# Kernel tuning notes

Hardware: AMD Instinct MI355X
Metric: run time of the kernel (lower is better)

## Reference

```python
import jax, jax.numpy as jnp
import numpy as np

V, D, H, L, T_MAX = 50257, 1024, 16, 12, 256
HS = D // H
B, T = 8, 256


def setup_inputs() -> dict:
    key = jax.random.key(0)
    ks = jax.random.split(key, 24)
    s = 0.02
    inp = {
        'idx': jax.random.randint(ks[0], (B, T), 0, V),
        'targets': jax.random.randint(ks[1], (B, T), 0, V),
        'tok_emb': jax.random.normal(ks[2], (V, D), jnp.float32) * s,
        'pos_emb': jax.random.normal(ks[3], (T_MAX, D), jnp.float32) * s,
        'Wq': jax.random.normal(ks[4], (L, H, D, HS), jnp.float32) / np.sqrt(D),
        'Wk': jax.random.normal(ks[5], (L, H, D, HS), jnp.float32) / np.sqrt(D),
        'Wv': jax.random.normal(ks[6], (L, H, D, HS), jnp.float32) / np.sqrt(D),
        'ln1_g': jnp.ones((L, D), jnp.float32),
        'ln1_b': jnp.zeros((L, D), jnp.float32),
        'ln2_g': jnp.ones((L, D), jnp.float32),
        'ln2_b': jnp.zeros((L, D), jnp.float32),
        'fc1_w': jax.random.normal(ks[7], (L, D, 4 * D), jnp.float32) / np.sqrt(D),
        'fc1_b': jnp.zeros((L, 4 * D), jnp.float32),
        'fc2_w': jax.random.normal(ks[8], (L, 4 * D, D), jnp.float32) / np.sqrt(4 * D),
        'fc2_b': jnp.zeros((L, D), jnp.float32),
        'lnf_g': jnp.ones((D,), jnp.float32),
        'lnf_b': jnp.zeros((D,), jnp.float32),
        'lm_w': jax.random.normal(ks[9], (D, V), jnp.float32) / np.sqrt(D),
        'lm_b': jnp.zeros((V,), jnp.float32),
    }
    return inp


def _layernorm(x, g, b, eps=1e-5):
    mu = jnp.mean(x, axis=-1, keepdims=True)
    var = jnp.var(x, axis=-1, keepdims=True)
    return (x - mu) * jax.lax.rsqrt(var + eps) * g + b


def reference(idx, targets, tok_emb, pos_emb, Wq, Wk, Wv, ln1_g, ln1_b, ln2_g, ln2_b,
              fc1_w, fc1_b, fc2_w, fc2_b, lnf_g, lnf_b, lm_w, lm_b):
    Bc, Tc = idx.shape
    x = tok_emb[idx] + pos_emb[:Tc]  # [B,T,D]
    causal = jnp.tril(jnp.ones((Tc, Tc), bool))
    scale = 1.0 / np.sqrt(HS)
    for l in range(L):
        h = _layernorm(x, ln1_g[l], ln1_b[l])
        q = jnp.einsum('btd,hds->bhts', h, Wq[l])
        k = jnp.einsum('btd,hds->bhts', h, Wk[l])
        v = jnp.einsum('btd,hds->bhts', h, Wv[l])
        scores = jnp.einsum('bhts,bhus->bhtu', q, k) * scale
        scores = jnp.where(causal, scores, -jnp.inf)
        attn = jax.nn.softmax(scores, axis=-1)
        o = jnp.einsum('bhtu,bhus->bhts', attn, v)  # [B,H,T,hs]
        o = o.transpose(0, 2, 1, 3).reshape(Bc, Tc, D)  # concat heads
        x = x + o  # no output projection in original
        h = _layernorm(x, ln2_g[l], ln2_b[l])
        ff = jax.nn.relu(h @ fc1_w[l] + fc1_b[l]) @ fc2_w[l] + fc2_b[l]
        x = x + ff
    x = _layernorm(x, lnf_g, lnf_b)
    logits = x @ lm_w + lm_b  # [B,T,V]
    logp = jax.nn.log_softmax(logits, axis=-1)
    nll = -jnp.take_along_axis(logp, targets[..., None], axis=-1)[..., 0]
    loss = jnp.mean(nll)
    return logits, loss
```

## Files before the change

### kernel.cpp

```cpp
#include <hip/hip_runtime.h>

#define T_SEQ 256
#define DMODEL 1024
#define NHEAD 16
#define HSZ 64
#define NLAYER 12
#define VOCAB 50257
#define NPAD 50304
#define FF 4096
#define MROWS 2048

using short8 = __attribute__((ext_vector_type(8))) short;
using f32x4  = __attribute__((ext_vector_type(4))) float;

__device__ __forceinline__ float bf2f(unsigned short u) {
    unsigned int x = ((unsigned int)u) << 16;
    return __builtin_bit_cast(float, x);
}
__device__ __forceinline__ unsigned short f2bf(float f) {
    unsigned int u = __builtin_bit_cast(unsigned int, f);
    unsigned int r = (u + 0x7fffu + ((u >> 16) & 1u)) >> 16;
    return (unsigned short)r;
}
__device__ __forceinline__ void async_copy16(const void* g, void* l) {
    __builtin_amdgcn_global_load_lds(
        (const __attribute__((address_space(1))) unsigned int*)g,
        (__attribute__((address_space(3))) unsigned int*)l, 16, 0, 0);
}

__device__ __forceinline__ void ln_tail(
    float4 v, const float* __restrict__ g, const float* __restrict__ b,
    int row, int tid, unsigned short* __restrict__ out)
{
    float s  = v.x + v.y + v.z + v.w;
    float ss = v.x * v.x + v.y * v.y + v.z * v.z + v.w * v.w;
    for (int o = 32; o > 0; o >>= 1) {
        s  += __shfl_down(s, o);
        ss += __shfl_down(ss, o);
    }
    __shared__ float ps[4], pss[4];
    int wave = tid >> 6, lane = tid & 63;
    if (lane == 0) { ps[wave] = s; pss[wave] = ss; }
    __syncthreads();
    float st  = ps[0] + ps[1] + ps[2] + ps[3];
    float sst = pss[0] + pss[1] + pss[2] + pss[3];
    float mu  = st * (1.0f / DMODEL);
    float var = sst * (1.0f / DMODEL) - mu * mu;
    float rstd = rsqrtf(var + 1e-5f);
    float4 gv = ((const float4*)g)[tid];
    float4 bv = ((const float4*)b)[tid];
    ushort4 o4;
    o4.x = f2bf((v.x - mu) * rstd * gv.x + bv.x);
    o4.y = f2bf((v.y - mu) * rstd * gv.y + bv.y);
    o4.z = f2bf((v.z - mu) * rstd * gv.z + bv.z);
    o4.w = f2bf((v.w - mu) * rstd * gv.w + bv.w);
    ((ushort4*)out)[(size_t)row * (DMODEL / 4) + tid] = o4;
}

__global__ __launch_bounds__(256) void embed_ln_kernel(
    const int* __restrict__ idx, const float* __restrict__ tok,
    const float* __restrict__ pos, const float* __restrict__ g,
    const float* __restrict__ b, float* __restrict__ x,
    unsigned short* __restrict__ h)
{
    int row = blockIdx.x, tid = threadIdx.x;
    int t = row & (T_SEQ - 1);
    int token = idx[row];
    float4 a = ((const float4*)(tok + (size_t)token * DMODEL))[tid];
    float4 p = ((const float4*)(pos + (size_t)t * DMODEL))[tid];
    float4 v;
    v.x = a.x + p.x; v.y = a.y + p.y; v.z = a.z + p.z; v.w = a.w + p.w;
    ((float4*)(x + (size_t)row * DMODEL))[tid] = v;
    ln_tail(v, g, b, row, tid, h);
}

__global__ __launch_bounds__(256) void ln_kernel(
    const float* __restrict__ x, const float* __restrict__ g,
    const float* __restrict__ b, unsigned short* __restrict__ out)
{
    int row = blockIdx.x, tid = threadIdx.x;
    float4 v = ((const float4*)(x + (size_t)row * DMODEL))[tid];
    ln_tail(v, g, b, row, tid, out);
}

__global__ __launch_bounds__(256) void fc2_merge_ln_kernel(
    const float* __restrict__ part, const float* __restrict__ bias,
    const float* __restrict__ g, const float* __restrict__ b,
    float* __restrict__ x, unsigned short* __restrict__ h)
{
    int row = blockIdx.x, tid = threadIdx.x;
    size_t o = (size_t)row * (DMODEL / 4) + tid;
    float4 p0 = ((const float4*)part)[o];
    float4 p1 = ((const float4*)part)[o + MROWS * (DMODEL / 4)];
    float4 bv = ((const float4*)bias)[tid];
    float4 v = ((float4*)x)[o];
    v.x += p0.x + p1.x + bv.x;
    v.y += p0.y + p1.y + bv.y;
    v.z += p0.z + p1.z + bv.z;
    v.w += p0.w + p1.w + bv.w;
    ((float4*)x)[o] = v;
    ln_tail(v, g, b, row, tid, h);
}

__global__ __launch_bounds__(256) void wtranspose_kernel(
    const float* __restrict__ in, unsigned short* __restrict__ out,
    int R, int C, int Cout, long in_l, long out_l)
{
    int lyr = blockIdx.z;
    in  += (size_t)lyr * in_l;
    out += (size_t)lyr * out_l;
    __shared__ float tile[32][33];
    int tx = threadIdx.x & 31, ty = threadIdx.x >> 5;
    int c0 = blockIdx.x * 32, r0 = blockIdx.y * 32;
    #pragma unroll
    for (int i = 0; i < 4; i++) {
        int r = r0 + ty + i * 8, c = c0 + tx;
        tile[ty + i * 8][tx] = (c < C) ? in[(size_t)r * C + c] : 0.f;
    }
    __syncthreads();
    #pragma unroll
    for (int i = 0; i < 4; i++) {
        int c = c0 + ty + i * 8, r = r0 + tx;
        if (c < Cout) out[(size_t)c * R + r] = f2bf(tile[tx][ty + i * 8]);
    }
}

__global__ __launch_bounds__(256) void qkvpack_kernel(
    const float* __restrict__ Wq, const float* __restrict__ Wk,
    const float* __restrict__ Wv, unsigned short* __restrict__ out,
    long w_l, long out_l)
{
    int z = blockIdx.z;
    int lyr = z / 48, r48 = z % 48;
    int seg = r48 >> 4, hh = r48 & 15;
    const float* W = (seg == 0 ? Wq : seg == 1 ? Wk : Wv)
                     + (size_t)lyr * w_l + (size_t)hh * DMODEL * HSZ;
    unsigned short* o = out + (size_t)lyr * out_l
                      + (size_t)(seg * 1024 + hh * 64) * DMODEL;
    __shared__ float tile[32][33];
    int tx = threadIdx.x & 31, ty = threadIdx.x >> 5;
    int d0 = blockIdx.x * 32, s0 = blockIdx.y * 32;
    #pragma unroll
    for (int i = 0; i < 4; i++)
        tile[ty + i * 8][tx] = W[(size_t)(d0 + ty + i * 8) * HSZ + s0 + tx];
    __syncthreads();
    #pragma unroll
    for (int i = 0; i < 4; i++)
        o[(size_t)(s0 + ty + i * 8) * DMODEL + d0 + tx] = f2bf(tile[tx][ty + i * 8]);
}

template<int MF, int WAVES, bool QKV, bool RELU, bool RES, bool CBF16>
__device__ __forceinline__ void gemm_core(
    const unsigned short* __restrict__ A, int lda,
    const unsigned short* __restrict__ Bt, int ldb,
    const float* __restrict__ bias,
    void* __restrict__ Cv, int ldc,
    const float* __restrict__ res, int ldr,
    int N, int K,
    unsigned short* __restrict__ vtout)
{
    constexpr int BM = (WAVES / 2) * MF * 16;
    constexpr int BJ = 16 / WAVES;
    __shared__ __align__(16) char As[BM * 128];
    __shared__ __align__(16) char Bs[128 * 128];
    int tid = threadIdx.x;
    int wave = tid >> 6, lane = tid & 63;
    int wr = wave >> 1, wc = wave & 1;
    int m0 = blockIdx.x * BM, n0 = blockIdx.y * 128;

    f32x4 acc[MF][4];
    #pragma unroll
    for (int m = 0; m < MF; m++)
        #pragma unroll
        for (int n = 0; n < 4; n++)
            acc[m][n] = (f32x4){0.f, 0.f, 0.f, 0.f};

    int ksw = (((lane & 7) ^ (lane >> 3)) << 4);
    int KT = K >> 6;
    for (int kt = 0; kt < KT; kt++) {
        int k0 = kt << 6;
        __syncthreads();
        #pragma unroll
        for (int j = 0; j < MF; j++) {
            int row = (wave * MF + j) * 8 + (lane >> 3);
            const char* src = (const char*)A + ((size_t)(m0 + row) * lda + k0) * 2 + ksw;
            async_copy16(src, As + (wave * MF + j) * 1024);
        }
        #pragma unroll
        for (int j = 0; j < BJ; j++) {
            int nrow = (wave * BJ + j) * 8 + (lane >> 3);
            const char* src = (const char*)Bt + ((size_t)(n0 + nrow) * ldb + k0) * 2 + ksw;
            async_copy16(src, Bs + (wave * BJ + j) * 1024);
        }
        __syncthreads();
        #pragma unroll
        for (int ks = 0; ks < 2; ks++) {
            int kb = ks * 64 + ((lane >> 4) << 4);
            short8 a[MF], b[4];
            #pragma unroll
            for (int m = 0; m < MF; m++) {
                int r = wr * (MF * 16) + m * 16 + (lane & 15);
                a[m] = *(const short8*)(const void*)(As + r * 128 + (kb ^ ((r & 7) << 4)));
            }
            #pragma unroll
            for (int n = 0; n < 4; n++) {
                int c = wc * 64 + n * 16 + (lane & 15);
                b[n] = *(const short8*)(const void*)(Bs + c * 128 + (kb ^ ((c & 7) << 4)));
            }
            #pragma unroll
            for (int m = 0; m < MF; m++)
                #pragma unroll
                for (int n = 0; n < 4; n++)
                    acc[m][n] = __builtin_amdgcn_mfma_f32_16x16x32_bf16(a[m], b[n], acc[m][n], 0, 0, 0);
        }
    }
    #pragma unroll
    for (int m = 0; m < MF; m++) {
        int rowb = m0 + wr * (MF * 16) + m * 16 + ((lane >> 4) << 2);
        #pragma unroll
        for (int n = 0; n < 4; n++) {
            int col = n0 + wc * 64 + n * 16 + (lane & 15);
            if (col < N) {
                float bi = bias ? bias[col] : 0.f;
                #pragma unroll
                for (int r2 = 0; r2 < 4; r2++) {
                    float v = acc[m][n][r2] + bi;
                    if (RELU) v = fmaxf(v, 0.f);
                    int row = rowb + r2;
                    if (RES) v += res[(size_t)row * ldr + col];
                    if (QKV && col >= 2048) {
                        int hh = (col - 2048) >> 6, sdim = (col - 2048) & 63;
                        int bb = row >> 8, tt = row & 255;
                        vtout[((((size_t)bb * NHEAD + hh) * HSZ + sdim) * T_SEQ) + tt] = f2bf(v);
                    } else if (CBF16) {
                        ((unsigned short*)Cv)[(size_t)row * ldc + col] = f2bf(v);
                    } else {
                        ((float*)Cv)[(size_t)row * ldc + col] = v;
                    }
                }
            }
        }
    }
}

__global__ __launch_bounds__(256) void gemm_qkv(
    const unsigned short* __restrict__ A, const unsigned short* __restrict__ Bt,
    unsigned short* __restrict__ C, unsigned short* __restrict__ vtout)
{
    gemm_core<4, 4, true, false, false, true>(
        A, DMODEL, Bt, DMODEL, nullptr, C, 3072, nullptr, 0, 3072, DMODEL, vtout);
}

__global__ __launch_bounds__(256) void gemm_fc1(
    const unsigned short* __restrict__ A, const unsigned short* __restrict__ Bt,
    const float* __restrict__ bias, unsigned short* __restrict__ C)
{
    gemm_core<4, 4, false, true, false, true>(
        A, DMODEL, Bt, DMODEL, bias, C, FF, nullptr, 0, FF, DMODEL, nullptr);
}

__global__ __launch_bounds__(256) void gemm_fc2(
    const unsigned short* __restrict__ A, const unsigned short* __restrict__ Bt,
    float* __restrict__ part)
{
    int z = blockIdx.z;
    gemm_core<2, 4, false, false, false, false>(
        A + z * 2048, FF, Bt + z * 2048, FF, nullptr,
        part + (size_t)z * MROWS * DMODEL, DMODEL, nullptr, 0,
        DMODEL, 2048, nullptr);
}

__global__ __launch_bounds__(512) void gemm_lm(
    const unsigned short* __restrict__ A, const unsigned short* __restrict__ Bt,
    const float* __restrict__ bias, float* __restrict__ C)
{
    gemm_core<4, 8, false, false, false, false>(
        A, DMODEL, Bt, DMODEL, bias, C, VOCAB, nullptr, 0, VOCAB, DMODEL, nullptr);
}

__global__ __launch_bounds__(256) void attn_fused_kernel(
    const unsigned short* __restrict__ qkv, const unsigned short* __restrict__ vt,
    float* __restrict__ x)
{
    int qt = blockIdx.x, hh = blockIdx.y, b = blockIdx.z;
    int tid = threadIdx.x;
    int wave = tid >> 6, lane = tid & 63;
    int g = lane >> 4, q = lane & 15;

    __shared__ __align__(16) char Kb[2][8192];
    __shared__ __align__(16) char Vb[2][8192];
    __shared__ __align__(16) char Plds[4][2048];

    int qrow = b * T_SEQ + qt * 64 + wave * 16 + q;
    const char* qp = (const char*)qkv + ((size_t)qrow * 3072 + hh * HSZ) * 2;
    short8 qreg[2];
    qreg[0] = *(const short8*)(const void*)(qp + (g << 4));
    qreg[1] = *(const short8*)(const void*)(qp + 64 + (g << 4));

    char* Pw = Plds[wave];

    f32x4 oacc[4];
    #pragma unroll
    for (int f = 0; f < 4; f++) oacc[f] = (f32x4){0.f, 0.f, 0.f, 0.f};
    float m_run = -1e30f, l_run = 0.f;

    int srow = wave * 8 + (lane >> 3);
    int sbyte = ((lane & 7) << 4) ^ ((srow & 7) << 4);

    auto stage = [&](int kt, int bi) {
        #pragma unroll
        for (int c = 0; c < 2; c++) {
            int row = c * 32 + srow;
            const char* src = (const char*)qkv +
                ((size_t)(b * T_SEQ + kt * 64 + row) * 3072 + 1024 + hh * HSZ) * 2 + sbyte;
            async_copy16(src, Kb[bi] + c * 4096 + wave * 1024);
        }
        #pragma unroll
        for (int c = 0; c < 2; c++) {
            int row = c * 32 + srow;
            const char* src = (const char*)vt +
                (((size_t)(b * NHEAD + hh) * HSZ + row) * T_SEQ + kt * 64) * 2 + sbyte;
            async_copy16(src, Vb[bi] + c * 4096 + wave * 1024);
        }
    };

    stage(0, 0);
    for (int kt = 0; kt <= qt; kt++) {
        int bi = kt & 1;
        __syncthreads();
        if (kt < qt) stage(kt + 1, bi ^ 1);

        f32x4 sacc[4];
        #pragma unroll
        for (int f = 0; f < 4; f++) sacc[f] = (f32x4){0.f, 0.f, 0.f, 0.f};
        #pragma unroll
        for (int ks = 0; ks < 2; ks++) {
            int kb = ks * 64 + (g << 4);
            #pragma unroll
            for (int f = 0; f < 4; f++) {
                int u = f * 16 + q;
                short8 kf = *(const short8*)(const void*)(Kb[bi] + u * 128 + (kb ^ ((u & 7) << 4)));
                sacc[f] = __builtin_amdgcn_mfma_f32_16x16x32_bf16(kf, qreg[ks], sacc[f], 0, 0, 0);
            }
        }
        float sv[4][4];
        #pragma unroll
        for (int f = 0; f < 4; f++)
            #pragma unroll
            for (int r = 0; r < 4; r++) {
                float v = sacc[f][r] * 0.125f;
                if (kt == qt) {
                    int u_loc = f * 16 + g * 4 + r;
                    if (u_loc > wave * 16 + q) v = -1e30f;
                }
                sv[f][r] = v;
            }
        float pm = -1e30f;
        #pragma unroll
        for (int f = 0; f < 4; f++)
            #pragma unroll
            for (int r = 0; r < 4; r++) pm = fmaxf(pm, sv[f][r]);
        pm = fmaxf(pm, __shfl_xor(pm, 16));
        pm = fmaxf(pm, __shfl_xor(pm, 32));
        float mnew = fmaxf(m_run, pm);
        float corr = __expf(m_run - mnew);
        float p[4][4];
        float ls = 0.f;
        #pragma unroll
        for (int f = 0; f < 4; f++)
            #pragma unroll
            for (int r = 0; r < 4; r++) {
                p[f][r] = __expf(sv[f][r] - mnew);
                ls += p[f][r];
            }
        ls += __shfl_xor(ls, 16);
        ls += __shfl_xor(ls, 32);
        l_run = l_run * corr + ls;
        m_run = mnew;
        #pragma unroll
        for (int r = 0; r < 4; r++) {
            float cr = __shfl(corr, (lane & 48) | (g * 4 + r));
            #pragma unroll
            for (int f = 0; f < 4; f++) oacc[f][r] *= cr;
        }
        #pragma unroll
        for (int f = 0; f < 4; f++)
            #pragma unroll
            for (int rp = 0; rp < 2; rp++) {
                int ue = f * 16 + g * 4 + rp * 2;
                unsigned int pk = (unsigned int)f2bf(p[f][rp * 2])
                                | ((unsigned int)f2bf(p[f][rp * 2 + 1]) << 16);
                *(unsigned int*)(void*)(Pw + q * 128 + ((ue * 2) ^ ((q & 7) << 4))) = pk;
            }
        #pragma unroll
        for (int ks = 0; ks < 2; ks++) {
            int kb = ks * 64 + (g << 4);
            short8 pa = *(const short8*)(const void*)(Pw + q * 128 + (kb ^ ((q & 7) << 4)));
            #pragma unroll
            for (int f = 0; f < 4; f++) {
                int s = f * 16 + q;
                short8 vf = *(const short8*)(const void*)(Vb[bi] + s * 128 + (kb ^ ((s & 7) << 4)));
                oacc[f] = __builtin_amdgcn_mfma_f32_16x16x32_bf16(pa, vf, oacc[f], 0, 0, 0);
            }
        }
    }
    float inv = 1.0f / l_run;
    #pragma unroll
    for (int r = 0; r < 4; r++) {
        float ir = __shfl(inv, (lane & 48) | (g * 4 + r));
        int row_g = b * T_SEQ + qt * 64 + wave * 16 + g * 4 + r;
        #pragma unroll
        for (int f = 0; f < 4; f++) {
            size_t xi = (size_t)row_g * DMODEL + hh * HSZ + f * 16 + q;
            x[xi] += oacc[f][r] * ir;
        }
    }
}

__global__ __launch_bounds__(256) void loss1_kernel(
    const float* __restrict__ logits, const int* __restrict__ targets,
    float* __restrict__ nll)
{
    int r = blockIdx.x, tid = threadIdx.x;
    const float* row = logits + (size_t)r * VOCAB;
    const float4* row4 = (const float4*)row;
    float m = -3.4e38f, s = 0.f;
    for (int v = tid; v < VOCAB / 4; v += 256) {
        float4 x4 = row4[v];
        float lm = fmaxf(fmaxf(x4.x, x4.y), fmaxf(x4.z, x4.w));
        float nm = fmaxf(m, lm);
        s = s * __expf(m - nm) + __expf(x4.x - nm) + __expf(x4.y - nm)
          + __expf(x4.z - nm) + __expf(x4.w - nm);
        m = nm;
    }
    if (tid == 0) {
        float xv = row[VOCAB - 1];
        float nm = fmaxf(m, xv);
        s = s * __expf(m - nm) + __expf(xv - nm);
        m = nm;
    }
    __shared__ float ms[256], ssh[256];
    ms[tid] = m; ssh[tid] = s;
    __syncthreads();
    for (int o = 128; o > 0; o >>= 1) {
        if (tid < o) {
            float m1 = ms[tid], s1 = ssh[tid];
            float m2 = ms[tid + o], s2 = ssh[tid + o];
            float nm = fmaxf(m1, m2);
            ssh[tid] = s1 * __expf(m1 - nm) + s2 * __expf(m2 - nm);
            ms[tid] = nm;
        }
        __syncthreads();
    }
    if (tid == 0) nll[r] = logf(ssh[0]) + ms[0] - row[targets[r]];
}

__global__ __launch_bounds__(256) void loss2_kernel(
    const float* __restrict__ nll, float* __restrict__ out)
{
    int tid = threadIdx.x;
    float s = 0.f;
    for (int i = tid; i < MROWS; i += 256) s += nll[i];
    __shared__ float red[256];
    red[tid] = s;
    __syncthreads();
    for (int o = 128; o > 0; o >>= 1) {
        if (tid < o) red[tid] += red[tid + o];
        __syncthreads();
    }
    if (tid == 0) out[0] = red[0] * (1.0f / MROWS);
}

extern "C" void kernel_launch(void* const* d_in, const int* in_sizes, int n_in,
                              void* d_out, int out_size, void* d_ws, size_t ws_size,
                              hipStream_t stream)
{
    const int*   idx  = (const int*)d_in[0];
    const int*   tgt  = (const int*)d_in[1];
    const float* tok  = (const float*)d_in[2];
    const float* pos  = (const float*)d_in[3];
    const float* Wq   = (const float*)d_in[4];
    const float* Wk   = (const float*)d_in[5];
    const float* Wv   = (const float*)d_in[6];
    const float* ln1g = (const float*)d_in[7];
    const float* ln1b = (const float*)d_in[8];
    const float* ln2g = (const float*)d_in[9];
    const float* ln2b = (const float*)d_in[10];
    const float* fc1w = (const float*)d_in[11];
    const float* fc1b = (const float*)d_in[12];
    const float* fc2w = (const float*)d_in[13];
    const float* fc2b = (const float*)d_in[14];
    const float* lnfg = (const float*)d_in[15];
    const float* lnfb = (const float*)d_in[16];
    const float* lmw  = (const float*)d_in[17];
    const float* lmb  = (const float*)d_in[18];

    char* ws = (char*)d_ws;
    float*          x    = (float*)(ws + 0);
    unsigned short* h    = (unsigned short*)(ws + 8388608);
    unsigned short* qkv  = (unsigned short*)(ws + 12582912);
    unsigned short* vt   = (unsigned short*)(ws + 25165824);
    unsigned short* mid  = (unsigned short*)(ws + 29360128);
    float*          nll  = (float*)(ws + 46137344);
    float*          fc2p = (float*)(ws + 46145536);
    unsigned short* lmwt = (unsigned short*)(ws + 62922752);
    const size_t UP_NEED = 442769408ull;
    bool upfront = (ws_size >= UP_NEED);
    unsigned short* qkvt = (unsigned short*)(ws + 165945344);
    unsigned short* fc1t, * fc2t;
    long qkvt_l, fc1t_l, fc2t_l;
    if (upfront) {
        fc1t = (unsigned short*)(ws + 241442816);
        fc2t = (unsigned short*)(ws + 342106112);
        qkvt_l = 3072 * 1024; fc1t_l = (long)FF * 1024; fc2t_l = (long)1024 * FF;
    } else {
        fc1t = (unsigned short*)(ws + 172236800);
        fc2t = (unsigned short*)(ws + 180625408);
        qkvt_l = 0; fc1t_l = 0; fc2t_l = 0;
    }
    float* logits = (float*)d_out;
    float* lossp  = logits + (size_t)MROWS * VOCAB;

    const long WQKV_L = (long)NHEAD * DMODEL * HSZ;
    if (upfront) {
        qkvpack_kernel<<<dim3(32, 2, 48 * NLAYER), 256, 0, stream>>>(
            Wq, Wk, Wv, qkvt, WQKV_L, qkvt_l);
        wtranspose_kernel<<<dim3(128, 32, NLAYER), 256, 0, stream>>>(
            fc1w, fc1t, DMODEL, FF, FF, (long)DMODEL * FF, fc1t_l);
        wtranspose_kernel<<<dim3(32, 128, NLAYER), 256, 0, stream>>>(
            fc2w, fc2t, FF, DMODEL, DMODEL, (long)FF * DMODEL, fc2t_l);
    }
    wtranspose_kernel<<<dim3(1572, 32, 1), 256, 0, stream>>>(
        lmw, lmwt, DMODEL, VOCAB, NPAD, 0, 0);

    embed_ln_kernel<<<MROWS, 256, 0, stream>>>(idx, tok, pos, ln1g, ln1b, x, h);

    for (int l = 0; l < NLAYER; l++) {
        unsigned short* qkvt_p = qkvt + (size_t)l * qkvt_l;
        unsigned short* fc1t_p = fc1t + (size_t)l * fc1t_l;
        unsigned short* fc2t_p = fc2t + (size_t)l * fc2t_l;
        if (!upfront) {
            qkvpack_kernel<<<dim3(32, 2, 48), 256, 0, stream>>>(
                Wq + (size_t)l * WQKV_L, Wk + (size_t)l * WQKV_L,
                Wv + (size_t)l * WQKV_L, qkvt, WQKV_L, 0);
            wtranspose_kernel<<<dim3(128, 32, 1), 256, 0, stream>>>(
                fc1w + (size_t)l * DMODEL * FF, fc1t, DMODEL, FF, FF, 0, 0);
            wtranspose_kernel<<<dim3(32, 128, 1), 256, 0, stream>>>(
                fc2w + (size_t)l * FF * DMODEL, fc2t, FF, DMODEL, DMODEL, 0, 0);
        }
        gemm_qkv<<<dim3(16, 24), 256, 0, stream>>>(h, qkvt_p, qkv, vt);
        attn_fused_kernel<<<dim3(4, NHEAD, 8), 256, 0, stream>>>(qkv, vt, x);
        ln_kernel<<<MROWS, 256, 0, stream>>>(x, ln2g + l * DMODEL, ln2b + l * DMODEL, h);
        gemm_fc1<<<dim3(16, 32), 256, 0, stream>>>(h, fc1t_p, fc1b + (size_t)l * FF, mid);
        gemm_fc2<<<dim3(32, 8, 2), 256, 0, stream>>>(mid, fc2t_p, fc2p);
        const float* ng = (l < NLAYER - 1) ? ln1g + (l + 1) * DMODEL : lnfg;
        const float* nb = (l < NLAYER - 1) ? ln1b + (l + 1) * DMODEL : lnfb;
        fc2_merge_ln_kernel<<<MROWS, 256, 0, stream>>>(
            fc2p, fc2b + (size_t)l * DMODEL, ng, nb, x, h);
    }

    gemm_lm<<<dim3(8, 393), 512, 0, stream>>>(h, lmwt, lmb, logits);

    loss1_kernel<<<MROWS, 256, 0, stream>>>(logits, tgt, nll);
    loss2_kernel<<<1, 256, 0, stream>>>(nll, lossp);
}
```

Baseline: 2.122 ms.

## Preload all K/V tiles in attention and vectorize transpose stores

The attention kernel now stages every causal K/V tile (up to four of 64 rows) into LDS at once with a single barrier, replacing the double-buffered per-iteration staging and its per-tile barriers. LDS use grows from 32KB to 72KB per block, which may reduce occupancy. The weight transpose and QKV pack kernels now write two bf16 values per store (ushort2) instead of one. Those kernels are likely setup-only.

```diff
diff --git a/kernel.cpp b/kernel.cpp
--- a/kernel.cpp
+++ b/kernel.cpp
@@ -118,10 +118,17 @@
         tile[ty + i * 8][tx] = (c < C) ? in[(size_t)r * C + c] : 0.f;
     }
     __syncthreads();
-    #pragma unroll
-    for (int i = 0; i < 4; i++) {
-        int c = c0 + ty + i * 8, r = r0 + tx;
-        if (c < Cout) out[(size_t)c * R + r] = f2bf(tile[tx][ty + i * 8]);
+    int wrl = (threadIdx.x & 15) * 2;
+    int wcl = threadIdx.x >> 4;
+    #pragma unroll
+    for (int i = 0; i < 2; i++) {
+        int c = c0 + wcl + i * 16, r = r0 + wrl;
+        if (c < Cout) {
+            ushort2 w;
+            w.x = f2bf(tile[wrl][wcl + i * 16]);
+            w.y = f2bf(tile[wrl + 1][wcl + i * 16]);
+            *(ushort2*)(out + (size_t)c * R + r) = w;
+        }
     }
 }
 
@@ -144,9 +151,16 @@
     for (int i = 0; i < 4; i++)
         tile[ty + i * 8][tx] = W[(size_t)(d0 + ty + i * 8) * HSZ + s0 + tx];
     __syncthreads();
-    #pragma unroll
-    for (int i = 0; i < 4; i++)
-        o[(size_t)(s0 + ty + i * 8) * DMODEL + d0 + tx] = f2bf(tile[tx][ty + i * 8]);
+    int wdl = (threadIdx.x & 15) * 2;
+    int wsl = threadIdx.x >> 4;
+    #pragma unroll
+    for (int i = 0; i < 2; i++) {
+        int s = s0 + wsl + i * 16, d = d0 + wdl;
+        ushort2 w;
+        w.x = f2bf(tile[wdl][wsl + i * 16]);
+        w.y = f2bf(tile[wdl + 1][wsl + i * 16]);
+        *(ushort2*)(o + (size_t)s * DMODEL + d) = w;
+    }
 }
 
 template<int MF, int WAVES, bool QKV, bool RELU, bool RES, bool CBF16>
@@ -287,8 +301,8 @@
     int wave = tid >> 6, lane = tid & 63;
     int g = lane >> 4, q = lane & 15;
 
-    __shared__ __align__(16) char Kb[2][8192];
-    __shared__ __align__(16) char Vb[2][8192];
+    __shared__ __align__(16) char Kb[4][8192];
+    __shared__ __align__(16) char Vb[4][8192];
     __shared__ __align__(16) char Plds[4][2048];
 
     int qrow = b * T_SEQ + qt * 64 + wave * 16 + q;
@@ -307,29 +321,25 @@
     int srow = wave * 8 + (lane >> 3);
     int sbyte = ((lane & 7) << 4) ^ ((srow & 7) << 4);
 
-    auto stage = [&](int kt, int bi) {
+    for (int kt = 0; kt <= qt; kt++) {
         #pragma unroll
         for (int c = 0; c < 2; c++) {
             int row = c * 32 + srow;
             const char* src = (const char*)qkv +
                 ((size_t)(b * T_SEQ + kt * 64 + row) * 3072 + 1024 + hh * HSZ) * 2 + sbyte;
-            async_copy16(src, Kb[bi] + c * 4096 + wave * 1024);
+            async_copy16(src, Kb[kt] + c * 4096 + wave * 1024);
         }
         #pragma unroll
         for (int c = 0; c < 2; c++) {
             int row = c * 32 + srow;
             const char* src = (const char*)vt +
                 (((size_t)(b * NHEAD + hh) * HSZ + row) * T_SEQ + kt * 64) * 2 + sbyte;
-            async_copy16(src, Vb[bi] + c * 4096 + wave * 1024);
-        }
-    };
-
-    stage(0, 0);
+            async_copy16(src, Vb[kt] + c * 4096 + wave * 1024);
+        }
+    }
+    __syncthreads();
+
     for (int kt = 0; kt <= qt; kt++) {
-        int bi = kt & 1;
-        __syncthreads();
-        if (kt < qt) stage(kt + 1, bi ^ 1);
-
         f32x4 sacc[4];
         #pragma unroll
         for (int f = 0; f < 4; f++) sacc[f] = (f32x4){0.f, 0.f, 0.f, 0.f};
@@ -339,7 +349,7 @@
             #pragma unroll
             for (int f = 0; f < 4; f++) {
                 int u = f * 16 + q;
-                short8 kf = *(const short8*)(const void*)(Kb[bi] + u * 128 + (kb ^ ((u & 7) << 4)));
+                short8 kf = *(const short8*)(const void*)(Kb[kt] + u * 128 + (kb ^ ((u & 7) << 4)));
                 sacc[f] = __builtin_amdgcn_mfma_f32_16x16x32_bf16(kf, qreg[ks], sacc[f], 0, 0, 0);
             }
         }
@@ -399,7 +409,7 @@
             #pragma unroll
             for (int f = 0; f < 4; f++) {
                 int s = f * 16 + q;
-                short8 vf = *(const short8*)(const void*)(Vb[bi] + s * 128 + (kb ^ ((s & 7) << 4)));
+                short8 vf = *(const short8*)(const void*)(Vb[kt] + s * 128 + (kb ^ ((s & 7) << 4)));
                 oacc[f] = __builtin_amdgcn_mfma_f32_16x16x32_bf16(pa, vf, oacc[f], 0, 0, 0);
             }
         }
```

New measurement: 2.120 ms. No clear change (-0.1%).
